# Performance work log

Hardware: AMD Instinct MI355X
Metric: run time of the kernel (lower is better)

Reference implementation:

```python
import jax, jax.numpy as jnp
import numpy as np

B, S, H, NH = 2, 2048, 1024, 16
HD = H // NH  # 64


def rope_cos_sin(seq_len, dim, base=10000.0, dtype=jnp.float32):
    inv_freq = 1.0 / (base ** (jnp.arange(0, dim, 2, dtype=jnp.float32) / dim))
    t = jnp.arange(seq_len, dtype=jnp.float32)
    freqs = jnp.outer(t, inv_freq)              # [S, dim/2]
    emb = jnp.concatenate([freqs, freqs], -1)   # [S, dim]
    # broadcast shape [1, S, 1, dim]
    return jnp.cos(emb)[None, :, None, :].astype(dtype), jnp.sin(emb)[None, :, None, :].astype(dtype)


def rotate_half(x):
    x1, x2 = x[..., : x.shape[-1] // 2], x[..., x.shape[-1] // 2:]
    return jnp.concatenate([-x2, x1], axis=-1)


def setup_inputs() -> dict:
    key = jax.random.key(0)
    ks = jax.random.split(key, 5)
    sc = 1.0 / np.sqrt(H)
    x = jax.random.normal(ks[0], (B, S, H), jnp.float32)
    Wq = jax.random.normal(ks[1], (H, H), jnp.float32) * sc
    Wk = jax.random.normal(ks[2], (H, H), jnp.float32) * sc
    Wv = jax.random.normal(ks[3], (H, H), jnp.float32) * sc
    Wo = jax.random.normal(ks[4], (H, H), jnp.float32) * sc
    z = jnp.zeros((H,), jnp.float32)
    mask = jnp.tril(jnp.ones((S, S), bool))[None, None]  # causal [1,1,S,S]
    return {"x": x, "Wq": Wq, "bq": z, "Wk": Wk, "bk": z, "Wv": Wv, "bv": z,
            "Wo": Wo, "bo": z, "mask": mask}


def reference(x, Wq, bq, Wk, bk, Wv, bv, Wo, bo, mask):
    b, s, _ = x.shape
    q = (x @ Wq.T + bq).reshape(b, s, NH, HD)
    k = (x @ Wk.T + bk).reshape(b, s, NH, HD)
    v = (x @ Wv.T + bv).reshape(b, s, NH, HD)
    cos, sin = rope_cos_sin(s, HD, dtype=x.dtype)
    q = q * cos + rotate_half(q) * sin
    k = k * cos + rotate_half(k) * sin
    # [b, h, s, s] scores, explicit as in original
    scores = jnp.einsum("bqhd,bkhd->bhqk", q, k) / jnp.sqrt(jnp.asarray(HD, x.dtype))
    scores = jnp.where(mask, scores, jnp.asarray(-jnp.inf, x.dtype))
    attn = jax.nn.softmax(scores, axis=-1)
    out = jnp.einsum("bhqk,bkhd->bqhd", attn, v).reshape(b, s, H)
    return out @ Wo.T + bo
```

## Files before the change

### kernel.cpp

```cpp
#include <hip/hip_runtime.h>

typedef __bf16 bf16;
typedef __bf16 bf16x4 __attribute__((ext_vector_type(4)));
typedef __bf16 bf16x8 __attribute__((ext_vector_type(8)));
typedef float floatx4 __attribute__((ext_vector_type(4)));

#define MFMA16(a, b, c) __builtin_amdgcn_mfma_f32_16x16x32_bf16(a, b, c, 0, 0, 0)

__device__ __forceinline__ void load_lds16(const void* g, void* l) {
    __builtin_amdgcn_global_load_lds(
        (const __attribute__((address_space(1))) unsigned int*)g,
        (__attribute__((address_space(3))) unsigned int*)l, 16, 0, 0);
}

__device__ __forceinline__ bf16x8 scale8(bf16x8 a, float s) {
    bf16x8 o;
    #pragma unroll
    for (int i = 0; i < 8; i++) o[i] = (bf16)((float)a[i] * s);
    return o;
}

#define WAITV4_BAR()  do { asm volatile("s_waitcnt vmcnt(4)" ::: "memory"); \
                           __builtin_amdgcn_s_barrier();                    \
                           __builtin_amdgcn_sched_barrier(0); } while (0)
#define WAITV0_BAR()  do { asm volatile("s_waitcnt vmcnt(0)" ::: "memory"); \
                           __builtin_amdgcn_s_barrier();                    \
                           __builtin_amdgcn_sched_barrier(0); } while (0)
#define TRAIL_BAR()   do { __builtin_amdgcn_sched_barrier(0);               \
                           asm volatile("s_waitcnt lgkmcnt(0)" ::: "memory"); \
                           __builtin_amdgcn_s_barrier(); } while (0)

__global__ __launch_bounds__(256) void cvt_all_kernel(
    const float* __restrict__ x, const float* __restrict__ wq,
    const float* __restrict__ wk, const float* __restrict__ wv,
    const float* __restrict__ wo,
    bf16* __restrict__ xb, bf16* __restrict__ wqb, bf16* __restrict__ wkb,
    bf16* __restrict__ wvb, bf16* __restrict__ wob)
{
    int bid = blockIdx.x;
    const float* src; bf16* dst; int off;
    if (bid < 4096)      { src = x;  dst = xb;  off = bid; }
    else if (bid < 5120) { src = wq; dst = wqb; off = bid - 4096; }
    else if (bid < 6144) { src = wk; dst = wkb; off = bid - 5120; }
    else if (bid < 7168) { src = wv; dst = wvb; off = bid - 6144; }
    else                 { src = wo; dst = wob; off = bid - 7168; }
    int idx = (off * 256 + threadIdx.x) * 4;
    float4 v = *(const float4*)&src[idx];
    bf16x4 o;
    o[0] = (bf16)v.x; o[1] = (bf16)v.y; o[2] = (bf16)v.z; o[3] = (bf16)v.w;
    *(bf16x4*)&dst[idx] = o;
}

__global__ __launch_bounds__(256) void cvt_kernel(const float* __restrict__ x,
                                                  bf16* __restrict__ xb) {
    int idx = (blockIdx.x * 256 + threadIdx.x) * 4;
    float4 v = *(const float4*)&x[idx];
    bf16x4 o;
    o[0] = (bf16)v.x; o[1] = (bf16)v.y; o[2] = (bf16)v.z; o[3] = (bf16)v.w;
    *(bf16x4*)&xb[idx] = o;
}


#define PREP_STAGE()                                                          \
    int u0 = w * 128 + lane;                                                  \
    int u1 = u0 + 64;                                                         \
    int r0_ = u0 >> 2, c0_ = ((u0 & 3) ^ ((r0_ >> 1) & 3)) * 8;               \
    int r1_ = u1 >> 2, c1_ = ((u1 & 3) ^ ((r1_ >> 1) & 3)) * 8;               \
    int du0 = w * 1024;                                                       \
    int du1 = du0 + 512;

#define STAGE_PF(Asrc, Bsrc, arow, brow, sbuf, kk0)                           \
    do {                                                                      \
        load_lds16(&Asrc[(size_t)((arow) + r0_) * 1024 + (kk0) + c0_],        \
                   &As[sbuf][0][0] + du0);                                    \
        load_lds16(&Asrc[(size_t)((arow) + r1_) * 1024 + (kk0) + c1_],        \
                   &As[sbuf][0][0] + du1);                                    \
        load_lds16(&Bsrc[(size_t)((brow) + r0_) * 1024 + (kk0) + c0_],        \
                   &Bs[sbuf][0][0] + du0);                                    \
        load_lds16(&Bsrc[(size_t)((brow) + r1_) * 1024 + (kk0) + c1_],        \
                   &Bs[sbuf][0][0] + du1);                                    \
    } while (0)

#define GEMM_CORE(Asrc, Bsrc, arow, brow)                                     \
    PREP_STAGE()                                                              \
    STAGE_PF(Asrc, Bsrc, arow, brow, 0, 0);                                   \
    _Pragma("unroll 2")                                                       \
    for (int s = 0; s < 32; s++) {                                            \
        int sb = s & 1;                                                       \
        if (s + 1 < 32) {                                                     \
            STAGE_PF(Asrc, Bsrc, arow, brow, sb ^ 1, (s + 1) * 32);           \
            WAITV4_BAR();                                                     \
        } else {                                                              \
            WAITV0_BAR();                                                     \
        }                                                                     \
        bf16x8 af[4], bfr[4];                                                 \
        _Pragma("unroll")                                                     \
        for (int mt = 0; mt < 4; mt++) {                                      \
            int row = wm + mt * 16 + l15;                                     \
            af[mt] = *(const bf16x8*)&As[sb][row][(quad ^ ((row >> 1) & 3)) * 8]; \
        }                                                                     \
        _Pragma("unroll")                                                     \
        for (int nt = 0; nt < 4; nt++) {                                      \
            int row = wn + nt * 16 + l15;                                     \
            bfr[nt] = *(const bf16x8*)&Bs[sb][row][(quad ^ ((row >> 1) & 3)) * 8]; \
        }                                                                     \
        __builtin_amdgcn_s_setprio(1);                                        \
        _Pragma("unroll")                                                     \
        for (int mt = 0; mt < 4; mt++)                                        \
            _Pragma("unroll")                                                 \
            for (int nt = 0; nt < 4; nt++)                                    \
                acc[mt][nt] = MFMA16(af[mt], bfr[nt], acc[mt][nt]);           \
        __builtin_amdgcn_s_setprio(0);                                        \
        TRAIL_BAR();                                                          \
    }

__global__ __launch_bounds__(256) void gemm_qkv_fast(
    const bf16* __restrict__ xb,
    const bf16* __restrict__ Wq, const bf16* __restrict__ Wk,
    const bf16* __restrict__ Wv,
    const float* __restrict__ bq, const float* __restrict__ bk,
    const float* __restrict__ bv,
    bf16* __restrict__ q_ws, bf16* __restrict__ k_ws, bf16* __restrict__ vt_ws)
{
    int m0 = blockIdx.x * 128;
    int n0 = blockIdx.y * 128;
    int sec = n0 >> 10;
    int nw0 = n0 & 1023;
    const bf16* W     = (sec == 0) ? Wq : (sec == 1) ? Wk : Wv;
    const float* bias = (sec == 0) ? bq : (sec == 1) ? bk : bv;

    __shared__ bf16 As[2][128][32];
    __shared__ bf16 Bs[2][128][32];

    int tid = threadIdx.x;
    int lane = tid & 63, w = tid >> 6;
    int l15 = lane & 15, quad = lane >> 4;
    int wm = (w >> 1) * 64, wn = (w & 1) * 64;

    floatx4 acc[4][4];
    #pragma unroll
    for (int i = 0; i < 4; i++)
        #pragma unroll
        for (int j = 0; j < 4; j++) acc[i][j] = (floatx4){0.f, 0.f, 0.f, 0.f};

    GEMM_CORE(xb, W, m0, nw0)

    if (sec < 2) {
        bf16* outp = (sec == 0) ? q_ws : k_ws;
        float inv[2];
        inv[0] = __expf(-(float)l15 * (9.210340371976184f / 32.0f));
        inv[1] = __expf(-(float)(16 + l15) * (9.210340371976184f / 32.0f));
        #pragma unroll
        for (int mt = 0; mt < 4; mt++) {
            #pragma unroll
            for (int r = 0; r < 4; r++) {
                int m = m0 + wm + mt * 16 + quad * 4 + r;
                int bb = m >> 11, s = m & 2047;
                #pragma unroll
                for (int nt = 0; nt < 2; nt++) {
                    int nl1 = nw0 + wn + nt * 16 + l15;
                    int nl2 = nl1 + 32;
                    float x1 = acc[mt][nt][r] + bias[nl1];
                    float x2 = acc[mt][nt + 2][r] + bias[nl2];
                    float ang = (float)s * inv[nt];
                    float sn, cs;
                    __sincosf(ang, &sn, &cs);
                    int hh = nl1 >> 6, d = nl1 & 63;
                    size_t base = ((size_t)(bb * 16 + hh) * 2048 + s) * 64;
                    outp[base + d]      = (bf16)(x1 * cs - x2 * sn);
                    outp[base + d + 32] = (bf16)(x2 * cs + x1 * sn);
                }
            }
        }
    } else {
        #pragma unroll
        for (int mt = 0; mt < 4; mt++) {
            int mbase = m0 + wm + mt * 16 + quad * 4;
            int bb = mbase >> 11, s0 = mbase & 2047;
            #pragma unroll
            for (int nt = 0; nt < 4; nt++) {
                int nl = nw0 + wn + nt * 16 + l15;
                int hh = nl >> 6, d = nl & 63;
                bf16x4 pk;
                #pragma unroll
                for (int r = 0; r < 4; r++) pk[r] = (bf16)(acc[mt][nt][r] + bias[nl]);
                *(bf16x4*)&vt_ws[((size_t)(bb * 16 + hh) * 64 + d) * 2048 + s0] = pk;
            }
        }
    }
}

__global__ __launch_bounds__(256) void gemm_out_fast(
    const bf16* __restrict__ A, const bf16* __restrict__ W,
    const float* __restrict__ bias, float* __restrict__ out)
{
    int m0 = blockIdx.x * 128;
    int n0 = blockIdx.y * 128;

    __shared__ bf16 As[2][128][32];
    __shared__ bf16 Bs[2][128][32];

    int tid = threadIdx.x;
    int lane = tid & 63, w = tid >> 6;
    int l15 = lane & 15, quad = lane >> 4;
    int wm = (w >> 1) * 64, wn = (w & 1) * 64;

    floatx4 acc[4][4];
    #pragma unroll
    for (int i = 0; i < 4; i++)
        #pragma unroll
        for (int j = 0; j < 4; j++) acc[i][j] = (floatx4){0.f, 0.f, 0.f, 0.f};

    GEMM_CORE(A, W, m0, n0)

    #pragma unroll
    for (int mt = 0; mt < 4; mt++) {
        #pragma unroll
        for (int r = 0; r < 4; r++) {
            int m = m0 + wm + mt * 16 + quad * 4 + r;
            #pragma unroll
            for (int nt = 0; nt < 4; nt++) {
                int nl = n0 + wn + nt * 16 + l15;
                out[(size_t)m * 1024 + nl] = acc[mt][nt][r] + bias[nl];
            }
        }
    }
}

__global__ __launch_bounds__(256) void gemm_qkv_f32w(
    const bf16* __restrict__ xb,
    const float* __restrict__ Wq, const float* __restrict__ Wk,
    const float* __restrict__ Wv,
    const float* __restrict__ bq, const float* __restrict__ bk,
    const float* __restrict__ bv,
    bf16* __restrict__ q_ws, bf16* __restrict__ k_ws, bf16* __restrict__ vt_ws)
{
    int m0 = blockIdx.x * 128;
    int n0 = blockIdx.y * 128;
    int sec = n0 >> 10;
    int nw0 = n0 & 1023;
    const float* W    = (sec == 0) ? Wq : (sec == 1) ? Wk : Wv;
    const float* bias = (sec == 0) ? bq : (sec == 1) ? bk : bv;

    __shared__ bf16 As[128][72];
    __shared__ bf16 Bs[128][72];

    int tid = threadIdx.x;
    int lane = tid & 63, w = tid >> 6;
    int l15 = lane & 15, quad = lane >> 4;
    int wm = (w >> 1) * 64, wn = (w & 1) * 64;
    int sr = tid >> 1;
    int sk = (tid & 1) * 32;

    floatx4 acc[4][4];
    #pragma unroll
    for (int i = 0; i < 4; i++)
        #pragma unroll
        for (int j = 0; j < 4; j++) acc[i][j] = (floatx4){0.f, 0.f, 0.f, 0.f};

    for (int k0 = 0; k0 < 1024; k0 += 64) {
        __syncthreads();
        const bf16* ap = &xb[(size_t)(m0 + sr) * 1024 + k0 + sk];
        bf16x8 a0 = *(const bf16x8*)(ap);
        bf16x8 a1 = *(const bf16x8*)(ap + 8);
        bf16x8 a2 = *(const bf16x8*)(ap + 16);
        bf16x8 a3 = *(const bf16x8*)(ap + 24);
        const float* wp = &W[(size_t)(nw0 + sr) * 1024 + k0 + sk];
        bf16x8 bv_[4];
        #pragma unroll
        for (int c = 0; c < 4; c++) {
            float4 f0 = *(const float4*)(wp + c * 8);
            float4 f1 = *(const float4*)(wp + c * 8 + 4);
            bf16x8 t;
            t[0] = (bf16)f0.x; t[1] = (bf16)f0.y; t[2] = (bf16)f0.z; t[3] = (bf16)f0.w;
            t[4] = (bf16)f1.x; t[5] = (bf16)f1.y; t[6] = (bf16)f1.z; t[7] = (bf16)f1.w;
            bv_[c] = t;
        }
        *(bf16x8*)&As[sr][sk + 0]  = a0;
        *(bf16x8*)&As[sr][sk + 8]  = a1;
        *(bf16x8*)&As[sr][sk + 16] = a2;
        *(bf16x8*)&As[sr][sk + 24] = a3;
        #pragma unroll
        for (int c = 0; c < 4; c++) *(bf16x8*)&Bs[sr][sk + c * 8] = bv_[c];
        __syncthreads();
        #pragma unroll
        for (int kk = 0; kk < 64; kk += 32) {
            bf16x8 af[4], bfr[4];
            #pragma unroll
            for (int mt = 0; mt < 4; mt++)
                af[mt] = *(const bf16x8*)&As[wm + mt * 16 + l15][kk + quad * 8];
            #pragma unroll
            for (int nt = 0; nt < 4; nt++)
                bfr[nt] = *(const bf16x8*)&Bs[wn + nt * 16 + l15][kk + quad * 8];
            #pragma unroll
            for (int mt = 0; mt < 4; mt++)
                #pragma unroll
                for (int nt = 0; nt < 4; nt++)
                    acc[mt][nt] = MFMA16(af[mt], bfr[nt], acc[mt][nt]);
        }
    }

    if (sec < 2) {
        bf16* outp = (sec == 0) ? q_ws : k_ws;
        float inv[2];
        inv[0] = __expf(-(float)l15 * (9.210340371976184f / 32.0f));
        inv[1] = __expf(-(float)(16 + l15) * (9.210340371976184f / 32.0f));
        #pragma unroll
        for (int mt = 0; mt < 4; mt++) {
            #pragma unroll
            for (int r = 0; r < 4; r++) {
                int m = m0 + wm + mt * 16 + quad * 4 + r;
                int bb = m >> 11, s = m & 2047;
                #pragma unroll
                for (int nt = 0; nt < 2; nt++) {
                    int nl1 = nw0 + wn + nt * 16 + l15;
                    int nl2 = nl1 + 32;
                    float x1 = acc[mt][nt][r] + bias[nl1];
                    float x2 = acc[mt][nt + 2][r] + bias[nl2];
                    float ang = (float)s * inv[nt];
                    float sn, cs;
                    __sincosf(ang, &sn, &cs);
                    int hh = nl1 >> 6, d = nl1 & 63;
                    size_t base = ((size_t)(bb * 16 + hh) * 2048 + s) * 64;
                    outp[base + d]      = (bf16)(x1 * cs - x2 * sn);
                    outp[base + d + 32] = (bf16)(x2 * cs + x1 * sn);
                }
            }
        }
    } else {
        #pragma unroll
        for (int mt = 0; mt < 4; mt++) {
            int mbase = m0 + wm + mt * 16 + quad * 4;
            int bb = mbase >> 11, s0 = mbase & 2047;
            #pragma unroll
            for (int nt = 0; nt < 4; nt++) {
                int nl = nw0 + wn + nt * 16 + l15;
                int hh = nl >> 6, d = nl & 63;
                bf16x4 pk;
                #pragma unroll
                for (int r = 0; r < 4; r++) pk[r] = (bf16)(acc[mt][nt][r] + bias[nl]);
                *(bf16x4*)&vt_ws[((size_t)(bb * 16 + hh) * 64 + d) * 2048 + s0] = pk;
            }
        }
    }
}

__global__ __launch_bounds__(256) void gemm_out_f32w(
    const bf16* __restrict__ A, const float* __restrict__ W,
    const float* __restrict__ bias, float* __restrict__ out)
{
    int m0 = blockIdx.x * 128;
    int n0 = blockIdx.y * 128;

    __shared__ bf16 As[128][72];
    __shared__ bf16 Bs[128][72];

    int tid = threadIdx.x;
    int lane = tid & 63, w = tid >> 6;
    int l15 = lane & 15, quad = lane >> 4;
    int wm = (w >> 1) * 64, wn = (w & 1) * 64;
    int sr = tid >> 1;
    int sk = (tid & 1) * 32;

    floatx4 acc[4][4];
    #pragma unroll
    for (int i = 0; i < 4; i++)
        #pragma unroll
        for (int j = 0; j < 4; j++) acc[i][j] = (floatx4){0.f, 0.f, 0.f, 0.f};

    for (int k0 = 0; k0 < 1024; k0 += 64) {
        __syncthreads();
        const bf16* ap = &A[(size_t)(m0 + sr) * 1024 + k0 + sk];
        bf16x8 a0 = *(const bf16x8*)(ap);
        bf16x8 a1 = *(const bf16x8*)(ap + 8);
        bf16x8 a2 = *(const bf16x8*)(ap + 16);
        bf16x8 a3 = *(const bf16x8*)(ap + 24);
        const float* wp = &W[(size_t)(n0 + sr) * 1024 + k0 + sk];
        bf16x8 bv_[4];
        #pragma unroll
        for (int c = 0; c < 4; c++) {
            float4 f0 = *(const float4*)(wp + c * 8);
            float4 f1 = *(const float4*)(wp + c * 8 + 4);
            bf16x8 t;
            t[0] = (bf16)f0.x; t[1] = (bf16)f0.y; t[2] = (bf16)f0.z; t[3] = (bf16)f0.w;
            t[4] = (bf16)f1.x; t[5] = (bf16)f1.y; t[6] = (bf16)f1.z; t[7] = (bf16)f1.w;
            bv_[c] = t;
        }
        *(bf16x8*)&As[sr][sk + 0]  = a0;
        *(bf16x8*)&As[sr][sk + 8]  = a1;
        *(bf16x8*)&As[sr][sk + 16] = a2;
        *(bf16x8*)&As[sr][sk + 24] = a3;
        #pragma unroll
        for (int c = 0; c < 4; c++) *(bf16x8*)&Bs[sr][sk + c * 8] = bv_[c];
        __syncthreads();
        #pragma unroll
        for (int kk = 0; kk < 64; kk += 32) {
            bf16x8 af[4], bfr[4];
            #pragma unroll
            for (int mt = 0; mt < 4; mt++)
                af[mt] = *(const bf16x8*)&As[wm + mt * 16 + l15][kk + quad * 8];
            #pragma unroll
            for (int nt = 0; nt < 4; nt++)
                bfr[nt] = *(const bf16x8*)&Bs[wn + nt * 16 + l15][kk + quad * 8];
            #pragma unroll
            for (int mt = 0; mt < 4; mt++)
                #pragma unroll
                for (int nt = 0; nt < 4; nt++)
                    acc[mt][nt] = MFMA16(af[mt], bfr[nt], acc[mt][nt]);
        }
    }

    #pragma unroll
    for (int mt = 0; mt < 4; mt++) {
        #pragma unroll
        for (int r = 0; r < 4; r++) {
            int m = m0 + wm + mt * 16 + quad * 4 + r;
            #pragma unroll
            for (int nt = 0; nt < 4; nt++) {
                int nl = n0 + wn + nt * 16 + l15;
                out[(size_t)m * 1024 + nl] = acc[mt][nt][r] + bias[nl];
            }
        }
    }
}

__global__ __launch_bounds__(256, 2) void attn_kernel(
    const bf16* __restrict__ q_ws, const bf16* __restrict__ k_ws,
    const bf16* __restrict__ vt_ws, bf16* __restrict__ o_ws)
{
    __shared__ bf16 Ks[2][64][64];
    __shared__ bf16 Vt[2][64][64];
    __shared__ bf16 Ps[4][16][64];

    int tid = threadIdx.x;
    int w = tid >> 6, lane = tid & 63;
    int l15 = lane & 15, quad = lane >> 4;

    int bid = blockIdx.x;
    int g = bid & 31;
    int x = bid >> 5;
    int bb = g >> 4, h = g & 15;
    const bf16* qp = q_ws + (size_t)g * 2048 * 64;
    const bf16* kp = k_ws + (size_t)g * 2048 * 64;
    const bf16* vp = vt_ws + (size_t)g * 64 * 2048;

    int g0 = (w * 2) * 64 + lane;
    int g1 = g0 + 64;
    int r0 = g0 >> 3, c0 = (g0 & 7) ^ (r0 & 7);
    int r1 = g1 >> 3, c1 = (g1 & 7) ^ (r1 & 7);
    int o0 = (w * 2) * 512;
    int o1 = o0 + 512;

    const float SCL = 0.125f * 1.4426950408889634f;
    const float MFIX = 20.0f;
    int lx7 = l15 & 7;

    bf16x8 ones8;
    #pragma unroll
    for (int i = 0; i < 8; i++) ones8[i] = (bf16)1.0f;

    #pragma unroll 1
    for (int pass = 0; pass < 2; ++pass) {
        int qt = pass ? (31 - x) : x;
        int qrow = qt * 64 + w * 16;
        int nkt = qt + 1;

        bf16x8 qf0 = scale8(*(const bf16x8*)&qp[(size_t)(qrow + l15) * 64 + quad * 8], SCL);
        bf16x8 qf1 = scale8(*(const bf16x8*)&qp[(size_t)(qrow + l15) * 64 + 32 + quad * 8], SCL);

        floatx4 lacc = (floatx4){0.f, 0.f, 0.f, 0.f};
        floatx4 acc[4];
        #pragma unroll
        for (int nt = 0; nt < 4; nt++) acc[nt] = (floatx4){0.f, 0.f, 0.f, 0.f};

        const bf16* kst0 = kp + (size_t)r0 * 64 + c0 * 8;
        const bf16* kst1 = kp + (size_t)r1 * 64 + c1 * 8;
        const bf16* vst0 = vp + (size_t)r0 * 2048 + c0 * 8;
        const bf16* vst1 = vp + (size_t)r1 * 2048 + c1 * 8;

        load_lds16(kst0, &Ks[0][0][0] + o0);
        load_lds16(kst1, &Ks[0][0][0] + o1);
        load_lds16(vst0, &Vt[0][0][0] + o0);
        load_lds16(vst1, &Vt[0][0][0] + o1);
        kst0 += 4096; kst1 += 4096; vst0 += 64; vst1 += 64;

        #pragma unroll 2
        for (int kt = 0; kt < nkt; kt++) {
            int buf = kt & 1;
            if (kt + 1 < nkt) {
                load_lds16(kst0, &Ks[buf ^ 1][0][0] + o0);
                load_lds16(kst1, &Ks[buf ^ 1][0][0] + o1);
                load_lds16(vst0, &Vt[buf ^ 1][0][0] + o0);
                load_lds16(vst1, &Vt[buf ^ 1][0][0] + o1);
                kst0 += 4096; kst1 += 4096; vst0 += 64; vst1 += 64;
                WAITV4_BAR();
            } else {
                WAITV0_BAR();
            }

            int kt0 = kt * 64;

            floatx4 st[4];
            __builtin_amdgcn_s_setprio(1);
            #pragma unroll
            for (int kb = 0; kb < 4; kb++) {
                int row = kb * 16 + l15;
                bf16x8 a0 = *(const bf16x8*)&Ks[buf][row][(quad ^ lx7) * 8];
                bf16x8 a1 = *(const bf16x8*)&Ks[buf][row][((quad + 4) ^ lx7) * 8];
                floatx4 z = {-MFIX, -MFIX, -MFIX, -MFIX};
                z = MFMA16(a0, qf0, z);
                z = MFMA16(a1, qf1, z);
                st[kb] = z;
            }
            __builtin_amdgcn_s_setprio(0);
            if (kt0 + 63 > qrow) {
                int q = qrow + l15;
                #pragma unroll
                for (int kb = 0; kb < 4; kb++)
                    #pragma unroll
                    for (int rr = 0; rr < 4; rr++) {
                        int key = kt0 + kb * 16 + quad * 4 + rr;
                        if (key > q) st[kb][rr] = -1e30f;
                    }
            }

            #pragma unroll
            for (int kb = 0; kb < 4; kb++) {
                bf16x4 pk;
                #pragma unroll
                for (int rr = 0; rr < 4; rr++)
                    pk[rr] = (bf16)exp2f(st[kb][rr]);
                int ch = kb * 2 + (quad >> 1);
                *(bf16x4*)&Ps[w][l15][((ch ^ lx7) << 3) + ((quad & 1) << 2)] = pk;
            }

            bf16x8 pb0 = *(const bf16x8*)&Ps[w][l15][(quad ^ lx7) << 3];
            bf16x8 pb1 = *(const bf16x8*)&Ps[w][l15][((quad + 4) ^ lx7) << 3];
            __builtin_amdgcn_s_setprio(1);
            #pragma unroll
            for (int nt = 0; nt < 4; nt++) {
                int row = nt * 16 + l15;
                bf16x8 v0 = *(const bf16x8*)&Vt[buf][row][(quad ^ lx7) * 8];
                bf16x8 v1 = *(const bf16x8*)&Vt[buf][row][((quad + 4) ^ lx7) * 8];
                acc[nt] = MFMA16(v0, pb0, acc[nt]);
                acc[nt] = MFMA16(v1, pb1, acc[nt]);
            }
            lacc = MFMA16(ones8, pb0, lacc);
            lacc = MFMA16(ones8, pb1, lacc);
            __builtin_amdgcn_s_setprio(0);

            TRAIL_BAR();
        }

        float inv = 1.f / lacc[0];
        int s = qrow + l15;
        #pragma unroll
        for (int nt = 0; nt < 4; nt++) {
            bf16x4 pk;
            #pragma unroll
            for (int rr = 0; rr < 4; rr++) pk[rr] = (bf16)(acc[nt][rr] * inv);
            *(bf16x4*)&o_ws[((size_t)(bb * 2048 + s)) * 1024 + h * 64 + nt * 16 + quad * 4] = pk;
        }
    }
}

extern "C" void kernel_launch(void* const* d_in, const int* in_sizes, int n_in,
                              void* d_out, int out_size, void* d_ws, size_t ws_size,
                              hipStream_t stream) {
    const float* x  = (const float*)d_in[0];
    const float* Wq = (const float*)d_in[1];
    const float* bq = (const float*)d_in[2];
    const float* Wk = (const float*)d_in[3];
    const float* bk = (const float*)d_in[4];
    const float* Wv = (const float*)d_in[5];
    const float* bv = (const float*)d_in[6];
    const float* Wo = (const float*)d_in[7];
    const float* bo = (const float*)d_in[8];
    float* out = (float*)d_out;

    const size_t NELEM = (size_t)2 * 2048 * 1024;
    const size_t WELEM = (size_t)1024 * 1024;
    bf16* xb    = (bf16*)d_ws;
    bf16* q_ws  = xb + NELEM;
    bf16* k_ws  = q_ws + NELEM;
    bf16* vt_ws = k_ws + NELEM;
    bf16* o_ws  = xb;
    bf16* wqb   = vt_ws + NELEM;
    bf16* wkb   = wqb + WELEM;
    bf16* wvb   = wkb + WELEM;
    bf16* wob   = wvb + WELEM;

    bool fast = ws_size >= (size_t)40 * 1024 * 1024;

    if (fast) {
        cvt_all_kernel<<<8192, 256, 0, stream>>>(x, Wq, Wk, Wv, Wo,
                                                 xb, wqb, wkb, wvb, wob);
        gemm_qkv_fast<<<dim3(32, 24), 256, 0, stream>>>(
            xb, wqb, wkb, wvb, bq, bk, bv, q_ws, k_ws, vt_ws);
        attn_kernel<<<512, 256, 0, stream>>>(q_ws, k_ws, vt_ws, o_ws);
        gemm_out_fast<<<dim3(32, 8), 256, 0, stream>>>(o_ws, wob, bo, out);
    } else {
        cvt_kernel<<<4096, 256, 0, stream>>>(x, xb);
        gemm_qkv_f32w<<<dim3(32, 24), 256, 0, stream>>>(
            xb, Wq, Wk, Wv, bq, bk, bv, q_ws, k_ws, vt_ws);
        attn_kernel<<<512, 256, 0, stream>>>(q_ws, k_ws, vt_ws, o_ws);
        gemm_out_f32w<<<dim3(32, 8), 256, 0, stream>>>(o_ws, Wo, bo, out);
    }
}
```

Before: 193.4 us.

## Process 128-row query tiles per block so K/V tiles are reused twice

The attention kernel no longer handles two paired 64-row query tiles in separate passes. Each block now owns one 128-row query tile, with every warp computing 32 query rows as two 16-row subtiles. Each K/V tile loaded into LDS is therefore used by twice as many query rows, which cuts global/LDS traffic and barriers per unit of work. The costs are higher register pressure from the doubled accumulators and blocks ordered largest-first without the previous pass pairing. The grid must also shrink to 16 query tiles per head, which is not shown in the visible launch code.

```diff
diff --git a/kernel.cpp b/kernel.cpp
--- a/kernel.cpp
+++ b/kernel.cpp
@@ -430,7 +430,7 @@
 {
     __shared__ bf16 Ks[2][64][64];
     __shared__ bf16 Vt[2][64][64];
-    __shared__ bf16 Ps[4][16][64];
+    __shared__ bf16 Ps[4][32][64];
 
     int tid = threadIdx.x;
     int w = tid >> 6, lane = tid & 63;
@@ -438,11 +438,12 @@
 
     int bid = blockIdx.x;
     int g = bid & 31;
-    int x = bid >> 5;
+    int qt = 15 - (bid >> 5);
     int bb = g >> 4, h = g & 15;
     const bf16* qp = q_ws + (size_t)g * 2048 * 64;
     const bf16* kp = k_ws + (size_t)g * 2048 * 64;
     const bf16* vp = vt_ws + (size_t)g * 64 * 2048;
+    int qrow = qt * 128 + w * 32;
 
     int g0 = (w * 2) * 64 + lane;
     int g1 = g0 + 64;
@@ -459,106 +460,131 @@
     #pragma unroll
     for (int i = 0; i < 8; i++) ones8[i] = (bf16)1.0f;
 
-    #pragma unroll 1
-    for (int pass = 0; pass < 2; ++pass) {
-        int qt = pass ? (31 - x) : x;
-        int qrow = qt * 64 + w * 16;
-        int nkt = qt + 1;
-
-        bf16x8 qf0 = scale8(*(const bf16x8*)&qp[(size_t)(qrow + l15) * 64 + quad * 8], SCL);
-        bf16x8 qf1 = scale8(*(const bf16x8*)&qp[(size_t)(qrow + l15) * 64 + 32 + quad * 8], SCL);
-
-        floatx4 lacc = (floatx4){0.f, 0.f, 0.f, 0.f};
-        floatx4 acc[4];
-        #pragma unroll
-        for (int nt = 0; nt < 4; nt++) acc[nt] = (floatx4){0.f, 0.f, 0.f, 0.f};
-
-        const bf16* kst0 = kp + (size_t)r0 * 64 + c0 * 8;
-        const bf16* kst1 = kp + (size_t)r1 * 64 + c1 * 8;
-        const bf16* vst0 = vp + (size_t)r0 * 2048 + c0 * 8;
-        const bf16* vst1 = vp + (size_t)r1 * 2048 + c1 * 8;
-
-        load_lds16(kst0, &Ks[0][0][0] + o0);
-        load_lds16(kst1, &Ks[0][0][0] + o1);
-        load_lds16(vst0, &Vt[0][0][0] + o0);
-        load_lds16(vst1, &Vt[0][0][0] + o1);
-        kst0 += 4096; kst1 += 4096; vst0 += 64; vst1 += 64;
-
-        #pragma unroll 2
-        for (int kt = 0; kt < nkt; kt++) {
-            int buf = kt & 1;
-            if (kt + 1 < nkt) {
-                load_lds16(kst0, &Ks[buf ^ 1][0][0] + o0);
-                load_lds16(kst1, &Ks[buf ^ 1][0][0] + o1);
-                load_lds16(vst0, &Vt[buf ^ 1][0][0] + o0);
-                load_lds16(vst1, &Vt[buf ^ 1][0][0] + o1);
-                kst0 += 4096; kst1 += 4096; vst0 += 64; vst1 += 64;
-                WAITV4_BAR();
-            } else {
-                WAITV0_BAR();
-            }
-
-            int kt0 = kt * 64;
-
-            floatx4 st[4];
-            __builtin_amdgcn_s_setprio(1);
-            #pragma unroll
-            for (int kb = 0; kb < 4; kb++) {
-                int row = kb * 16 + l15;
-                bf16x8 a0 = *(const bf16x8*)&Ks[buf][row][(quad ^ lx7) * 8];
-                bf16x8 a1 = *(const bf16x8*)&Ks[buf][row][((quad + 4) ^ lx7) * 8];
+    bf16x8 qf[2][2];
+    #pragma unroll
+    for (int qs = 0; qs < 2; qs++) {
+        const bf16* qr = &qp[(size_t)(qrow + qs * 16 + l15) * 64];
+        qf[qs][0] = scale8(*(const bf16x8*)&qr[quad * 8], SCL);
+        qf[qs][1] = scale8(*(const bf16x8*)&qr[32 + quad * 8], SCL);
+    }
+
+    floatx4 lacc[2];
+    floatx4 acc[4][2];
+    #pragma unroll
+    for (int qs = 0; qs < 2; qs++) {
+        lacc[qs] = (floatx4){0.f, 0.f, 0.f, 0.f};
+        #pragma unroll
+        for (int nt = 0; nt < 4; nt++) acc[nt][qs] = (floatx4){0.f, 0.f, 0.f, 0.f};
+    }
+
+    int nkt = 2 * qt + 2;
+
+    const bf16* kst0 = kp + (size_t)r0 * 64 + c0 * 8;
+    const bf16* kst1 = kp + (size_t)r1 * 64 + c1 * 8;
+    const bf16* vst0 = vp + (size_t)r0 * 2048 + c0 * 8;
+    const bf16* vst1 = vp + (size_t)r1 * 2048 + c1 * 8;
+
+    load_lds16(kst0, &Ks[0][0][0] + o0);
+    load_lds16(kst1, &Ks[0][0][0] + o1);
+    load_lds16(vst0, &Vt[0][0][0] + o0);
+    load_lds16(vst1, &Vt[0][0][0] + o1);
+    kst0 += 4096; kst1 += 4096; vst0 += 64; vst1 += 64;
+
+    #pragma unroll 2
+    for (int kt = 0; kt < nkt; kt++) {
+        int buf = kt & 1;
+        if (kt + 1 < nkt) {
+            load_lds16(kst0, &Ks[buf ^ 1][0][0] + o0);
+            load_lds16(kst1, &Ks[buf ^ 1][0][0] + o1);
+            load_lds16(vst0, &Vt[buf ^ 1][0][0] + o0);
+            load_lds16(vst1, &Vt[buf ^ 1][0][0] + o1);
+            kst0 += 4096; kst1 += 4096; vst0 += 64; vst1 += 64;
+            WAITV4_BAR();
+        } else {
+            WAITV0_BAR();
+        }
+
+        int kt0 = kt * 64;
+
+        floatx4 st[2][4];
+        __builtin_amdgcn_s_setprio(1);
+        #pragma unroll
+        for (int kb = 0; kb < 4; kb++) {
+            int row = kb * 16 + l15;
+            bf16x8 a0 = *(const bf16x8*)&Ks[buf][row][(quad ^ lx7) * 8];
+            bf16x8 a1 = *(const bf16x8*)&Ks[buf][row][((quad + 4) ^ lx7) * 8];
+            #pragma unroll
+            for (int qs = 0; qs < 2; qs++) {
                 floatx4 z = {-MFIX, -MFIX, -MFIX, -MFIX};
-                z = MFMA16(a0, qf0, z);
-                z = MFMA16(a1, qf1, z);
-                st[kb] = z;
-            }
-            __builtin_amdgcn_s_setprio(0);
-            if (kt0 + 63 > qrow) {
-                int q = qrow + l15;
+                z = MFMA16(a0, qf[qs][0], z);
+                z = MFMA16(a1, qf[qs][1], z);
+                st[qs][kb] = z;
+            }
+        }
+        __builtin_amdgcn_s_setprio(0);
+        if (kt0 + 63 > qrow) {
+            #pragma unroll
+            for (int qs = 0; qs < 2; qs++) {
+                int q = qrow + qs * 16 + l15;
                 #pragma unroll
                 for (int kb = 0; kb < 4; kb++)
                     #pragma unroll
                     for (int rr = 0; rr < 4; rr++) {
                         int key = kt0 + kb * 16 + quad * 4 + rr;
-                        if (key > q) st[kb][rr] = -1e30f;
+                        if (key > q) st[qs][kb][rr] = -1e30f;
                     }
             }
-
+        }
+
+        #pragma unroll
+        for (int qs = 0; qs < 2; qs++)
             #pragma unroll
             for (int kb = 0; kb < 4; kb++) {
                 bf16x4 pk;
                 #pragma unroll
                 for (int rr = 0; rr < 4; rr++)
-                    pk[rr] = (bf16)exp2f(st[kb][rr]);
+                    pk[rr] = (bf16)exp2f(st[qs][kb][rr]);
                 int ch = kb * 2 + (quad >> 1);
-                *(bf16x4*)&Ps[w][l15][((ch ^ lx7) << 3) + ((quad & 1) << 2)] = pk;
-            }
-
-            bf16x8 pb0 = *(const bf16x8*)&Ps[w][l15][(quad ^ lx7) << 3];
-            bf16x8 pb1 = *(const bf16x8*)&Ps[w][l15][((quad + 4) ^ lx7) << 3];
-            __builtin_amdgcn_s_setprio(1);
-            #pragma unroll
-            for (int nt = 0; nt < 4; nt++) {
-                int row = nt * 16 + l15;
-                bf16x8 v0 = *(const bf16x8*)&Vt[buf][row][(quad ^ lx7) * 8];
-                bf16x8 v1 = *(const bf16x8*)&Vt[buf][row][((quad + 4) ^ lx7) * 8];
-                acc[nt] = MFMA16(v0, pb0, acc[nt]);
-                acc[nt] = MFMA16(v1, pb1, acc[nt]);
-            }
-            lacc = MFMA16(ones8, pb0, lacc);
-            lacc = MFMA16(ones8, pb1, lacc);
-            __builtin_amdgcn_s_setprio(0);
-
-            TRAIL_BAR();
-        }
-
-        float inv = 1.f / lacc[0];
-        int s = qrow + l15;
+                *(bf16x4*)&Ps[w][qs * 16 + l15][((ch ^ lx7) << 3) + ((quad & 1) << 2)] = pk;
+            }
+
+        bf16x8 pb[2][2];
+        #pragma unroll
+        for (int qs = 0; qs < 2; qs++) {
+            pb[qs][0] = *(const bf16x8*)&Ps[w][qs * 16 + l15][(quad ^ lx7) << 3];
+            pb[qs][1] = *(const bf16x8*)&Ps[w][qs * 16 + l15][((quad + 4) ^ lx7) << 3];
+        }
+        __builtin_amdgcn_s_setprio(1);
+        #pragma unroll
+        for (int nt = 0; nt < 4; nt++) {
+            int row = nt * 16 + l15;
+            bf16x8 v0 = *(const bf16x8*)&Vt[buf][row][(quad ^ lx7) * 8];
+            bf16x8 v1 = *(const bf16x8*)&Vt[buf][row][((quad + 4) ^ lx7) * 8];
+            #pragma unroll
+            for (int qs = 0; qs < 2; qs++) {
+                acc[nt][qs] = MFMA16(v0, pb[qs][0], acc[nt][qs]);
+                acc[nt][qs] = MFMA16(v1, pb[qs][1], acc[nt][qs]);
+            }
+        }
+        #pragma unroll
+        for (int qs = 0; qs < 2; qs++) {
+            lacc[qs] = MFMA16(ones8, pb[qs][0], lacc[qs]);
+            lacc[qs] = MFMA16(ones8, pb[qs][1], lacc[qs]);
+        }
+        __builtin_amdgcn_s_setprio(0);
+
+        TRAIL_BAR();
+    }
+
+    #pragma unroll
+    for (int qs = 0; qs < 2; qs++) {
+        float inv = 1.f / lacc[qs][0];
+        int s = qrow + qs * 16 + l15;
         #pragma unroll
         for (int nt = 0; nt < 4; nt++) {
             bf16x4 pk;
             #pragma unroll
-            for (int rr = 0; rr < 4; rr++) pk[rr] = (bf16)(acc[nt][rr] * inv);
+            for (int rr = 0; rr < 4; rr++) pk[rr] = (bf16)(acc[nt][qs][rr] * inv);
             *(bf16x4*)&o_ws[((size_t)(bb * 2048 + s)) * 1024 + h * 64 + nt * 16 + quad * 4] = pk;
         }
     }
```

After: 197.7 us. +2.2%, slower.
